# Kernel tuning notes

Measured on AMD Instinct MI355X. Metric: run time of the kernel, lower is better.

Reference implementation:

```python
import jax, jax.numpy as jnp
import numpy as np

N = 50000      # nodes
E = 800000     # edges (avg degree 16)
DIN = 128
DH = 128
DOUT = 40
ALPHA = 0.1
BETA = 1.0


def gcn_conv(x, src, dst, ew, W, b, n):
    """PyG GCNConv: add self-loops, symmetric deg^-1/2 normalization, gather-scatter."""
    idx = jnp.arange(n)
    s = jnp.concatenate([src, idx])
    d = jnp.concatenate([dst, idx])
    w = jnp.concatenate([ew, jnp.ones((n,), x.dtype)])
    deg = jax.ops.segment_sum(w, d, num_segments=n)            # [N]
    dinv = jnp.where(deg > 0, jax.lax.rsqrt(deg), 0.0)
    norm = dinv[s] * w * dinv[d]                               # [E+N]
    h = x @ W                                                  # [N, dout]
    msg = h[s] * norm[:, None]                                 # gather + scale
    out = jax.ops.segment_sum(msg, d, num_segments=n)          # scatter-add
    return out + b


def setup_inputs() -> dict:
    key = jax.random.key(0)
    ks = jax.random.split(key, 10)
    x = jax.random.normal(ks[0], (N, DIN), jnp.float32)
    edge_index = jax.random.randint(ks[1], (2, E), 0, N, dtype=jnp.int64)
    edge_weight = jax.random.uniform(ks[2], (E,), jnp.float32)
    W1 = jax.random.normal(ks[3], (DIN, DH), jnp.float32) / np.float32(np.sqrt(DIN))
    b1 = jnp.zeros((DH,), jnp.float32)
    W2 = jax.random.normal(ks[4], (DH, DH), jnp.float32) / np.float32(np.sqrt(DH))
    b2 = jnp.zeros((DH,), jnp.float32)
    W3 = jax.random.normal(ks[5], (DH, DOUT), jnp.float32) / np.float32(np.sqrt(DH))
    b3 = jnp.zeros((DOUT,), jnp.float32)
    return {"x": x, "edge_index": edge_index, "edge_weight": edge_weight,
            "W1": W1, "b1": b1, "W2": W2, "b2": b2, "W3": W3, "b3": b3}


def reference(x, edge_index, edge_weight, W1, b1, W2, b2, W3, b3):
    src, dst = edge_index[0], edge_index[1]
    ones_w = jnp.ones((E,), x.dtype)
    h1 = jax.nn.relu(gcn_conv(x, src, dst, ones_w, W1, b1, N))   # conv1 (edge_weight=None)
    hc = gcn_conv(h1, src, dst, edge_weight, W2, b2, N)          # crf_layer with edge_weight
    h = ALPHA * h1 + BETA * hc                                   # weighted residual combo
    # LearnableBernoulliDropout: identity in eval mode
    out = gcn_conv(h, src, dst, ones_w, W3, b3, N)               # conv2
    return jax.nn.log_softmax(out, axis=1)
```

## Files before the change

kernel.cpp:

```cpp
#include <hip/hip_runtime.h>
#include <math.h>

#define DIN  128
#define DH   128
#define DOUT 40
#define ALPHA_C 0.1f
#define BETA_C  1.0f
#define NXCD 8
#define PSLOT 16
#define FSLOT 64

typedef __attribute__((ext_vector_type(8))) short short8;
typedef __attribute__((ext_vector_type(4))) float floatx4;

static inline int cdiv_h(int a, int b) { return (a + b - 1) / b; }

static __device__ __forceinline__ unsigned short f2b(float f) {
    unsigned u = __float_as_uint(f);
    u = u + 0x7FFFu + ((u >> 16) & 1u);
    return (unsigned short)(u >> 16);
}
static __device__ __forceinline__ unsigned pk2(float x, float y) {
    return (unsigned)f2b(x) | ((unsigned)f2b(y) << 16);
}
static __device__ __forceinline__ float2 b2f2(unsigned u) {
    float2 r;
    r.x = __uint_as_float(u << 16);
    r.y = __uint_as_float(u & 0xFFFF0000u);
    return r;
}

__global__ __launch_bounds__(256) void build_part(const int* __restrict__ src,
                                                  const int* __restrict__ dst,
                                                  const float* __restrict__ ew,
                                                  int* __restrict__ cnt8,
                                                  int2* __restrict__ csrP, int N, int E) {
    unsigned xcc = __builtin_amdgcn_s_getreg((31u << 11) | 20u) & 7u;
    int quarter = (E + 3) >> 2;
    int e0 = blockIdx.x * 256 + threadIdx.x;
    int* cntp = cnt8 + (size_t)xcc * N;

    int idx[4]; int d[4], s[4]; float w[4]; int pos[4]; bool v[4];
    #pragma unroll
    for (int k = 0; k < 4; ++k) { idx[k] = e0 + k * quarter; v[k] = idx[k] < E; }
    #pragma unroll
    for (int k = 0; k < 4; ++k) if (v[k]) { d[k] = dst[idx[k]]; s[k] = src[idx[k]]; w[k] = ew[idx[k]]; }
    #pragma unroll
    for (int k = 0; k < 4; ++k) if (v[k])
        pos[k] = __hip_atomic_fetch_add(&cntp[d[k]], 1, __ATOMIC_RELAXED, __HIP_MEMORY_SCOPE_WORKGROUP);
    #pragma unroll
    for (int k = 0; k < 4; ++k) if (v[k] && pos[k] < PSLOT - 1) {
        int2 r; r.x = s[k]; r.y = __float_as_int(w[k]);
        csrP[((size_t)d[k] << 7) + (xcc << 4) + pos[k]] = r;
    }
}

__global__ __launch_bounds__(256) void compact(const int* __restrict__ cnt8,
                                               const int2* __restrict__ csrP,
                                               int2* __restrict__ csrF,
                                               int* __restrict__ len,
                                               float* __restrict__ dinv1,
                                               float* __restrict__ dinv2, int N) {
    int row = blockIdx.x * 4 + (threadIdx.x >> 6);
    if (row >= N) return;
    int lane = threadIdx.x & 63;

    int cg[NXCD], pre[NXCD]; int tot = 0;
    #pragma unroll
    for (int g = 0; g < NXCD; ++g) {
        int c = cnt8[(size_t)g * N + row];
        if (c > PSLOT - 1) c = PSLOT - 1;
        cg[g] = c; pre[g] = tot; tot += c;
    }

    float wsum = 0.f;
    #pragma unroll
    for (int h = 0; h < 2; ++h) {
        int slot = lane + 64 * h;
        int g = slot >> 4, pos = slot & 15;
        if (pos < cg[g]) {
            int2 r = csrP[((size_t)row << 7) + slot];
            int dsti = pre[g] + pos;
            if (dsti < FSLOT) csrF[((size_t)row << 6) + dsti] = r;
            wsum += __int_as_float(r.y);
        }
    }
    #pragma unroll
    for (int o = 1; o < 64; o <<= 1) wsum += __shfl_xor(wsum, o, 64);

    if (lane == 0) {
        int t = tot > FSLOT ? FSLOT : tot;
        len[row] = t;
        dinv1[row] = rsqrtf((float)tot + 1.f);
        dinv2[row] = rsqrtf(wsum + 1.f);
    }
}

__global__ __launch_bounds__(256) void wt_conv(const float* __restrict__ W1,
                                               const float* __restrict__ W2,
                                               const float* __restrict__ W3,
                                               unsigned short* __restrict__ WT) {
    int gid = blockIdx.x * 256 + threadIdx.x;
    if (gid < 16384) {
        int n = gid >> 7, k = gid & 127;
        WT[gid] = f2b(W1[(size_t)k * 128 + n]);
    } else if (gid < 32768) {
        int idx = gid - 16384, n = idx >> 7, k = idx & 127;
        WT[gid] = f2b(W2[(size_t)k * 128 + n]);
    } else if (gid < 32768 + 6144) {
        int idx = gid - 32768, n = idx >> 7, k = idx & 127;
        WT[gid] = (n < 40) ? f2b(W3[(size_t)k * 40 + n]) : (unsigned short)0;
    }
}

template <bool ABF16>
__global__ __launch_bounds__(256) void gemm128(const void* __restrict__ Ain,
                                               const unsigned short* __restrict__ WT,
                                               unsigned short* __restrict__ C, int M) {
    __shared__ short As[128 * 128];
    __shared__ short Bs[128 * 128];
    int t = threadIdx.x;
    int blockM = blockIdx.x * 128;
    int r = t >> 1, h = t & 1;

    {
        int rg = blockM + r; if (rg > M - 1) rg = M - 1;
        if (ABF16) {
            const uint4* arow = (const uint4*)((const unsigned short*)Ain + (size_t)rg * 128);
            #pragma unroll
            for (int i = 0; i < 8; ++i) {
                int chunk = h * 8 + i;
                uint4 v = arow[chunk];
                *(uint4*)&As[r * 128 + ((chunk ^ (r & 7)) * 8)] = v;
            }
        } else {
            const float4* arow = (const float4*)((const float*)Ain + (size_t)rg * 128);
            #pragma unroll
            for (int i = 0; i < 8; ++i) {
                int chunk = h * 8 + i;
                float4 v0 = arow[chunk * 2], v1 = arow[chunk * 2 + 1];
                uint4 p;
                p.x = pk2(v0.x, v0.y); p.y = pk2(v0.z, v0.w);
                p.z = pk2(v1.x, v1.y); p.w = pk2(v1.z, v1.w);
                *(uint4*)&As[r * 128 + ((chunk ^ (r & 7)) * 8)] = p;
            }
        }
    }
    {
        const uint4* brow = (const uint4*)(WT + (size_t)r * 128);
        #pragma unroll
        for (int i = 0; i < 8; ++i) {
            int chunk = h * 8 + i;
            uint4 v = brow[chunk];
            *(uint4*)&Bs[r * 128 + ((chunk ^ (r & 7)) * 8)] = v;
        }
    }
    __syncthreads();

    int w = t >> 6, l = t & 63;
    int q = l >> 4, lm = l & 15;
    int rowoff = (w >> 1) * 64, coloff = (w & 1) * 64;

    floatx4 acc[4][4] = {};
    #pragma unroll
    for (int ks = 0; ks < 4; ++ks) {
        int chunk = ks * 4 + q;
        int sw = (chunk ^ (lm & 7)) * 8;
        short8 af[4], bf[4];
        #pragma unroll
        for (int tm = 0; tm < 4; ++tm)
            af[tm] = *(const short8*)&As[(rowoff + tm * 16 + lm) * 128 + sw];
        #pragma unroll
        for (int tn = 0; tn < 4; ++tn)
            bf[tn] = *(const short8*)&Bs[(coloff + tn * 16 + lm) * 128 + sw];
        #pragma unroll
        for (int tm = 0; tm < 4; ++tm)
            #pragma unroll
            for (int tn = 0; tn < 4; ++tn)
                acc[tm][tn] = __builtin_amdgcn_mfma_f32_16x16x32_bf16(af[tm], bf[tn], acc[tm][tn], 0, 0, 0);
    }

    #pragma unroll
    for (int tm = 0; tm < 4; ++tm) {
        #pragma unroll
        for (int reg = 0; reg < 4; ++reg) {
            int row = blockM + rowoff + tm * 16 + q * 4 + reg;
            if (row >= M) continue;
            #pragma unroll
            for (int tn = 0; tn < 4; ++tn) {
                int col = coloff + tn * 16 + lm;
                C[(size_t)row * 128 + col] = f2b(acc[tm][tn][reg]);
            }
        }
    }
}

__global__ __launch_bounds__(256) void gemm40_lsm(const unsigned short* __restrict__ Ain,
                                                  const unsigned short* __restrict__ WT3,
                                                  const float* __restrict__ bias,
                                                  float* __restrict__ out, int M) {
    __shared__ short As[128 * 128];
    __shared__ short Bs[48 * 128];
    int t = threadIdx.x;
    int blockM = blockIdx.x * 128;

    {
        int r = t >> 1, h = t & 1;
        int rg = blockM + r; if (rg > M - 1) rg = M - 1;
        const uint4* arow = (const uint4*)(Ain + (size_t)rg * 128);
        #pragma unroll
        for (int i = 0; i < 8; ++i) {
            int chunk = h * 8 + i;
            uint4 v = arow[chunk];
            *(uint4*)&As[r * 128 + ((chunk ^ (r & 7)) * 8)] = v;
        }
    }
    if (t < 96) {
        int r = t >> 1, h = t & 1;
        const uint4* brow = (const uint4*)(WT3 + (size_t)r * 128);
        #pragma unroll
        for (int i = 0; i < 8; ++i) {
            int chunk = h * 8 + i;
            uint4 v = brow[chunk];
            *(uint4*)&Bs[r * 128 + ((chunk ^ (r & 7)) * 8)] = v;
        }
    }
    __syncthreads();

    int w = t >> 6, l = t & 63;
    int q = l >> 4, lm = l & 15;
    int rowoff = w * 32;

    floatx4 acc[2][3] = {};
    #pragma unroll
    for (int ks = 0; ks < 4; ++ks) {
        int chunk = ks * 4 + q;
        int sw = (chunk ^ (lm & 7)) * 8;
        short8 af[2], bf[3];
        #pragma unroll
        for (int tm = 0; tm < 2; ++tm)
            af[tm] = *(const short8*)&As[(rowoff + tm * 16 + lm) * 128 + sw];
        #pragma unroll
        for (int tn = 0; tn < 3; ++tn)
            bf[tn] = *(const short8*)&Bs[(tn * 16 + lm) * 128 + sw];
        #pragma unroll
        for (int tm = 0; tm < 2; ++tm)
            #pragma unroll
            for (int tn = 0; tn < 3; ++tn)
                acc[tm][tn] = __builtin_amdgcn_mfma_f32_16x16x32_bf16(af[tm], bf[tn], acc[tm][tn], 0, 0, 0);
    }

    float bb0 = bias[lm];
    float bb1 = bias[16 + lm];
    float bb2 = (lm < 8) ? bias[32 + lm] : 0.f;
    #pragma unroll
    for (int tm = 0; tm < 2; ++tm) {
        #pragma unroll
        for (int reg = 0; reg < 4; ++reg) {
            int row = blockM + rowoff + tm * 16 + q * 4 + reg;
            float v0 = acc[tm][0][reg] + bb0;
            float v1 = acc[tm][1][reg] + bb1;
            float v2 = (lm < 8) ? acc[tm][2][reg] + bb2 : -INFINITY;
            float mx = fmaxf(fmaxf(v0, v1), v2);
            #pragma unroll
            for (int o = 1; o < 16; o <<= 1) mx = fmaxf(mx, __shfl_xor(mx, o, 64));
            float ss = expf(v0 - mx) + expf(v1 - mx) + ((lm < 8) ? expf(v2 - mx) : 0.f);
            #pragma unroll
            for (int o = 1; o < 16; o <<= 1) ss += __shfl_xor(ss, o, 64);
            float ls = mx + logf(ss);
            if (row < M) {
                out[(size_t)row * 40 + lm]      = v0 - ls;
                out[(size_t)row * 40 + 16 + lm] = v1 - ls;
                if (lm < 8) out[(size_t)row * 40 + 32 + lm] = v2 - ls;
            }
        }
    }
}

template <int MODE>
__global__ __launch_bounds__(256) void agg128f(const unsigned short* __restrict__ hpre,
                                               unsigned short* __restrict__ io,
                                               const float* __restrict__ bias,
                                               const float* __restrict__ dinv,
                                               const int* __restrict__ len,
                                               const int2* __restrict__ csrF, int n) {
    int row = blockIdx.x * 4 + (threadIdx.x >> 6);
    if (row >= n) return;
    int lane = threadIdx.x & 63;
    const unsigned* hp = (const unsigned*)hpre;

    float di = dinv[row];
    float d2 = di * di;
    float2 acc = b2f2(hp[(size_t)row * 64 + lane]);
    if (MODE == 2) {
        acc.x *= d2; acc.y *= d2;
    } else {
        float2 bb = ((const float2*)bias)[lane];
        acc.x = fmaf(acc.x, d2, bb.x);
        acc.y = fmaf(acc.y, d2, bb.y);
    }

    int c = len[row];
    size_t jb = (size_t)row << 6;
    int j = 0;

    while (j + 8 <= c) {
        int2 ee[8]; float2 ff[8];
        #pragma unroll
        for (int u = 0; u < 8; ++u) ee[u] = csrF[jb + j + u];
        #pragma unroll
        for (int u = 0; u < 8; ++u) ff[u] = b2f2(hp[(size_t)ee[u].x * 64 + lane]);
        #pragma unroll
        for (int u = 0; u < 8; ++u) {
            float cc = (MODE == 1) ? dinv[ee[u].x] * __int_as_float(ee[u].y) * di
                                   : dinv[ee[u].x] * di;
            acc.x = fmaf(cc, ff[u].x, acc.x);
            acc.y = fmaf(cc, ff[u].y, acc.y);
        }
        j += 8;
    }
    if (j + 4 <= c) {
        int2 ee[4]; float2 ff[4];
        #pragma unroll
        for (int u = 0; u < 4; ++u) ee[u] = csrF[jb + j + u];
        #pragma unroll
        for (int u = 0; u < 4; ++u) ff[u] = b2f2(hp[(size_t)ee[u].x * 64 + lane]);
        #pragma unroll
        for (int u = 0; u < 4; ++u) {
            float cc = (MODE == 1) ? dinv[ee[u].x] * __int_as_float(ee[u].y) * di
                                   : dinv[ee[u].x] * di;
            acc.x = fmaf(cc, ff[u].x, acc.x);
            acc.y = fmaf(cc, ff[u].y, acc.y);
        }
        j += 4;
    }
    for (; j < c; ++j) {
        int2 e0 = csrF[jb + j];
        float cc = (MODE == 1) ? dinv[e0.x] * __int_as_float(e0.y) * di : dinv[e0.x] * di;
        float2 f0 = b2f2(hp[(size_t)e0.x * 64 + lane]);
        acc.x = fmaf(cc, f0.x, acc.x);
        acc.y = fmaf(cc, f0.y, acc.y);
    }

    unsigned* iop = (unsigned*)io;
    if (MODE == 0) {
        acc.x = fmaxf(acc.x, 0.f); acc.y = fmaxf(acc.y, 0.f);
        iop[(size_t)row * 64 + lane] = pk2(acc.x, acc.y);
    } else if (MODE == 1) {
        float2 h1 = b2f2(iop[(size_t)row * 64 + lane]);
        acc.x = fmaf(ALPHA_C, h1.x, BETA_C * acc.x);
        acc.y = fmaf(ALPHA_C, h1.y, BETA_C * acc.y);
        iop[(size_t)row * 64 + lane] = pk2(acc.x, acc.y);
    } else {
        iop[(size_t)row * 64 + lane] = pk2(acc.x, acc.y);
    }
}

extern "C" void kernel_launch(void* const* d_in, const int* in_sizes, int n_in,
                              void* d_out, int out_size, void* d_ws, size_t ws_size,
                              hipStream_t stream) {
    const float* x   = (const float*)d_in[0];
    const int*   ei  = (const int*)  d_in[1];
    const float* ew  = (const float*)d_in[2];
    const float* W1  = (const float*)d_in[3];
    const float* b1  = (const float*)d_in[4];
    const float* W2  = (const float*)d_in[5];
    const float* b2  = (const float*)d_in[6];
    const float* W3  = (const float*)d_in[7];
    const float* b3  = (const float*)d_in[8];
    float* out = (float*)d_out;

    const int Nn = in_sizes[0] / DIN;
    const int E  = in_sizes[1] / 2;
    const int* src = ei;
    const int* dst = ei + E;

    char* wsb = (char*)d_ws;
    int*      cnt8  = (int*)wsb;                         wsb += (size_t)NXCD * Nn * 4;
    int*      len   = (int*)wsb;                         wsb += (size_t)Nn * 4;
    float*    dinv1 = (float*)wsb;                       wsb += (size_t)Nn * 4;
    float*    dinv2 = (float*)wsb;                       wsb += (size_t)Nn * 4;
    unsigned short* WT = (unsigned short*)wsb;           wsb += (size_t)(32768 + 6144) * 2;
    int2*     csrF  = (int2*)wsb;                        wsb += (size_t)Nn * FSLOT * 8;
    int2*     csrP  = (int2*)wsb;
    unsigned short* hpreb = (unsigned short*)csrP;
    unsigned short* h1b   = (unsigned short*)csrP + (size_t)Nn * DH;

    hipMemsetAsync(cnt8, 0, (size_t)NXCD * Nn * 4, stream);
    build_part<<<cdiv_h((E + 3) / 4, 256), 256, 0, stream>>>(src, dst, ew, cnt8, csrP, Nn, E);
    compact<<<cdiv_h(Nn, 4), 256, 0, stream>>>(cnt8, csrP, csrF, len, dinv1, dinv2, Nn);
    wt_conv<<<cdiv_h(32768 + 6144, 256), 256, 0, stream>>>(W1, W2, W3, WT);

    int gemmGrid = cdiv_h(Nn, 128);
    int aggGrid = cdiv_h(Nn, 4);

    gemm128<false><<<gemmGrid, 256, 0, stream>>>(x, WT, hpreb, Nn);
    agg128f<0><<<aggGrid, 256, 0, stream>>>(hpreb, h1b, b1, dinv1, len, csrF, Nn);

    gemm128<true><<<gemmGrid, 256, 0, stream>>>(h1b, WT + 16384, hpreb, Nn);
    agg128f<1><<<aggGrid, 256, 0, stream>>>(hpreb, h1b, b2, dinv2, len, csrF, Nn);

    agg128f<2><<<aggGrid, 256, 0, stream>>>(h1b, hpreb, b3, dinv1, len, csrF, Nn);
    gemm40_lsm<<<gemmGrid, 256, 0, stream>>>(hpreb, WT + 32768, b3, out, Nn);
}
```

Baseline: 306.3 us.

## Pack CSR edges to 32-bit, fuse setup kernels, and split rows across half-waves

Each edge record is packed into one 32-bit word: a 16-bit source index plus a bf16 edge weight. This halves the CSR bytes written and read. The weight-transpose kernel is merged into the edge-partition kernel, and the compaction pass is merged into the first GEMM launch as extra blocks, which removes two launches and lets independent work overlap. The aggregation kernel now has each half-wave handle alternate edges with 8-byte feature loads, then combines the halves with a cross-lane shuffle. The 16-bit source index only works while N is at most 65536, and the bf16 weight lowers precision in the CRF normalization.

```diff
diff --git a/kernel.cpp b/kernel.cpp
--- a/kernel.cpp
+++ b/kernel.cpp
@@ -9,6 +9,7 @@
 #define NXCD 8
 #define PSLOT 16
 #define FSLOT 64
+#define WT_TOT (16384 + 16384 + 6144)
 
 typedef __attribute__((ext_vector_type(8))) short short8;
 typedef __attribute__((ext_vector_type(4))) float floatx4;
@@ -30,99 +31,57 @@
     return r;
 }
 
-__global__ __launch_bounds__(256) void build_part(const int* __restrict__ src,
-                                                  const int* __restrict__ dst,
-                                                  const float* __restrict__ ew,
-                                                  int* __restrict__ cnt8,
-                                                  int2* __restrict__ csrP, int N, int E) {
+__global__ __launch_bounds__(256) void build_wt(const int* __restrict__ src,
+                                                const int* __restrict__ dst,
+                                                const float* __restrict__ ew,
+                                                const float* __restrict__ W1,
+                                                const float* __restrict__ W2,
+                                                const float* __restrict__ W3,
+                                                int* __restrict__ cnt8,
+                                                unsigned* __restrict__ csrP,
+                                                unsigned short* __restrict__ WT,
+                                                int N, int E, int buildBlocks) {
+    int b = blockIdx.x;
+    if (b >= buildBlocks) {
+        int gid = (b - buildBlocks) * 256 + threadIdx.x;
+        if (gid < 16384) {
+            int n = gid >> 7, k = gid & 127;
+            WT[gid] = f2b(W1[(size_t)k * 128 + n]);
+        } else if (gid < 32768) {
+            int idx = gid - 16384, n = idx >> 7, k = idx & 127;
+            WT[gid] = f2b(W2[(size_t)k * 128 + n]);
+        } else if (gid < WT_TOT) {
+            int idx = gid - 32768, n = idx >> 7, k = idx & 127;
+            WT[gid] = (n < 40) ? f2b(W3[(size_t)k * 40 + n]) : (unsigned short)0;
+        }
+        return;
+    }
     unsigned xcc = __builtin_amdgcn_s_getreg((31u << 11) | 20u) & 7u;
     int quarter = (E + 3) >> 2;
-    int e0 = blockIdx.x * 256 + threadIdx.x;
+    int e0 = b * 256 + threadIdx.x;
     int* cntp = cnt8 + (size_t)xcc * N;
 
-    int idx[4]; int d[4], s[4]; float w[4]; int pos[4]; bool v[4];
+    int idx[4], d[4]; unsigned rec[4]; int pos[4]; bool v[4];
     #pragma unroll
     for (int k = 0; k < 4; ++k) { idx[k] = e0 + k * quarter; v[k] = idx[k] < E; }
     #pragma unroll
-    for (int k = 0; k < 4; ++k) if (v[k]) { d[k] = dst[idx[k]]; s[k] = src[idx[k]]; w[k] = ew[idx[k]]; }
+    for (int k = 0; k < 4; ++k) if (v[k]) {
+        d[k] = dst[idx[k]];
+        rec[k] = ((unsigned)f2b(ew[idx[k]]) << 16) | ((unsigned)src[idx[k]] & 0xFFFFu);
+    }
     #pragma unroll
     for (int k = 0; k < 4; ++k) if (v[k])
         pos[k] = __hip_atomic_fetch_add(&cntp[d[k]], 1, __ATOMIC_RELAXED, __HIP_MEMORY_SCOPE_WORKGROUP);
     #pragma unroll
-    for (int k = 0; k < 4; ++k) if (v[k] && pos[k] < PSLOT - 1) {
-        int2 r; r.x = s[k]; r.y = __float_as_int(w[k]);
-        csrP[((size_t)d[k] << 7) + (xcc << 4) + pos[k]] = r;
-    }
-}
-
-__global__ __launch_bounds__(256) void compact(const int* __restrict__ cnt8,
-                                               const int2* __restrict__ csrP,
-                                               int2* __restrict__ csrF,
-                                               int* __restrict__ len,
-                                               float* __restrict__ dinv1,
-                                               float* __restrict__ dinv2, int N) {
-    int row = blockIdx.x * 4 + (threadIdx.x >> 6);
-    if (row >= N) return;
-    int lane = threadIdx.x & 63;
-
-    int cg[NXCD], pre[NXCD]; int tot = 0;
-    #pragma unroll
-    for (int g = 0; g < NXCD; ++g) {
-        int c = cnt8[(size_t)g * N + row];
-        if (c > PSLOT - 1) c = PSLOT - 1;
-        cg[g] = c; pre[g] = tot; tot += c;
-    }
-
-    float wsum = 0.f;
-    #pragma unroll
-    for (int h = 0; h < 2; ++h) {
-        int slot = lane + 64 * h;
-        int g = slot >> 4, pos = slot & 15;
-        if (pos < cg[g]) {
-            int2 r = csrP[((size_t)row << 7) + slot];
-            int dsti = pre[g] + pos;
-            if (dsti < FSLOT) csrF[((size_t)row << 6) + dsti] = r;
-            wsum += __int_as_float(r.y);
-        }
-    }
-    #pragma unroll
-    for (int o = 1; o < 64; o <<= 1) wsum += __shfl_xor(wsum, o, 64);
-
-    if (lane == 0) {
-        int t = tot > FSLOT ? FSLOT : tot;
-        len[row] = t;
-        dinv1[row] = rsqrtf((float)tot + 1.f);
-        dinv2[row] = rsqrtf(wsum + 1.f);
-    }
-}
-
-__global__ __launch_bounds__(256) void wt_conv(const float* __restrict__ W1,
-                                               const float* __restrict__ W2,
-                                               const float* __restrict__ W3,
-                                               unsigned short* __restrict__ WT) {
-    int gid = blockIdx.x * 256 + threadIdx.x;
-    if (gid < 16384) {
-        int n = gid >> 7, k = gid & 127;
-        WT[gid] = f2b(W1[(size_t)k * 128 + n]);
-    } else if (gid < 32768) {
-        int idx = gid - 16384, n = idx >> 7, k = idx & 127;
-        WT[gid] = f2b(W2[(size_t)k * 128 + n]);
-    } else if (gid < 32768 + 6144) {
-        int idx = gid - 32768, n = idx >> 7, k = idx & 127;
-        WT[gid] = (n < 40) ? f2b(W3[(size_t)k * 40 + n]) : (unsigned short)0;
-    }
+    for (int k = 0; k < 4; ++k) if (v[k] && pos[k] < PSLOT - 1)
+        csrP[((size_t)d[k] << 7) + (xcc << 4) + pos[k]] = rec[k];
 }
 
 template <bool ABF16>
-__global__ __launch_bounds__(256) void gemm128(const void* __restrict__ Ain,
-                                               const unsigned short* __restrict__ WT,
-                                               unsigned short* __restrict__ C, int M) {
-    __shared__ short As[128 * 128];
-    __shared__ short Bs[128 * 128];
-    int t = threadIdx.x;
-    int blockM = blockIdx.x * 128;
+static __device__ __forceinline__ void gemm128_body(short* As, short* Bs,
+        const void* __restrict__ Ain, const unsigned short* __restrict__ WT,
+        unsigned short* __restrict__ C, int M, int blockM, int t) {
     int r = t >> 1, h = t & 1;
-
     {
         int rg = blockM + r; if (rg > M - 1) rg = M - 1;
         if (ABF16) {
@@ -195,6 +154,64 @@
     }
 }
 
+template <bool ABF16>
+__global__ __launch_bounds__(256) void gemm128(const void* __restrict__ Ain,
+                                               const unsigned short* __restrict__ WT,
+                                               unsigned short* __restrict__ C, int M) {
+    __shared__ short As[128 * 128];
+    __shared__ short Bs[128 * 128];
+    gemm128_body<ABF16>(As, Bs, Ain, WT, C, M, blockIdx.x * 128, threadIdx.x);
+}
+
+__global__ __launch_bounds__(256) void gemm1_compact(const float* __restrict__ x,
+                                                     const unsigned short* __restrict__ WT,
+                                                     unsigned short* __restrict__ C, int M,
+                                                     const int* __restrict__ cnt8,
+                                                     const unsigned* __restrict__ csrP,
+                                                     unsigned* __restrict__ csrF,
+                                                     int* __restrict__ len,
+                                                     float* __restrict__ dinv1,
+                                                     float* __restrict__ dinv2,
+                                                     int N, int gemmBlocks) {
+    __shared__ short As[128 * 128];
+    __shared__ short Bs[128 * 128];
+    if ((int)blockIdx.x < gemmBlocks) {
+        gemm128_body<false>(As, Bs, x, WT, C, M, blockIdx.x * 128, threadIdx.x);
+        return;
+    }
+    int bid = blockIdx.x - gemmBlocks;
+    int row = bid * 4 + (threadIdx.x >> 6);
+    if (row >= N) return;
+    int lane = threadIdx.x & 63;
+
+    int cg[NXCD], pre[NXCD]; int tot = 0;
+    #pragma unroll
+    for (int g = 0; g < NXCD; ++g) {
+        int c = cnt8[(size_t)g * N + row];
+        if (c > PSLOT - 1) c = PSLOT - 1;
+        cg[g] = c; pre[g] = tot; tot += c;
+    }
+    float wsum = 0.f;
+    #pragma unroll
+    for (int h2 = 0; h2 < 2; ++h2) {
+        int slot = lane + 64 * h2;
+        int g = slot >> 4, pos = slot & 15;
+        if (pos < cg[g]) {
+            unsigned rec = csrP[((size_t)row << 7) + slot];
+            int dsti = pre[g] + pos;
+            if (dsti < FSLOT) csrF[((size_t)row << 6) + dsti] = rec;
+            wsum += __uint_as_float(rec & 0xFFFF0000u);
+        }
+    }
+    #pragma unroll
+    for (int o = 1; o < 64; o <<= 1) wsum += __shfl_xor(wsum, o, 64);
+    if (lane == 0) {
+        len[row] = tot > FSLOT ? FSLOT : tot;
+        dinv1[row] = rsqrtf((float)tot + 1.f);
+        dinv2[row] = rsqrtf(wsum + 1.f);
+    }
+}
+
 __global__ __launch_bounds__(256) void gemm40_lsm(const unsigned short* __restrict__ Ain,
                                                   const unsigned short* __restrict__ WT3,
                                                   const float* __restrict__ bias,
@@ -278,81 +295,95 @@
 }
 
 template <int MODE>
+static __device__ __forceinline__ void edge_acc(unsigned e, uint2 v, float di,
+                                                const float* __restrict__ dinv, float4& acc) {
+    int s = e & 0xFFFFu;
+    float cc = (MODE == 1) ? dinv[s] * __uint_as_float(e & 0xFFFF0000u) * di
+                           : dinv[s] * di;
+    float2 p0 = b2f2(v.x), p1 = b2f2(v.y);
+    acc.x = fmaf(cc, p0.x, acc.x); acc.y = fmaf(cc, p0.y, acc.y);
+    acc.z = fmaf(cc, p1.x, acc.z); acc.w = fmaf(cc, p1.y, acc.w);
+}
+
+template <int MODE>
 __global__ __launch_bounds__(256) void agg128f(const unsigned short* __restrict__ hpre,
                                                unsigned short* __restrict__ io,
                                                const float* __restrict__ bias,
                                                const float* __restrict__ dinv,
                                                const int* __restrict__ len,
-                                               const int2* __restrict__ csrF, int n) {
+                                               const unsigned* __restrict__ csrF, int n) {
     int row = blockIdx.x * 4 + (threadIdx.x >> 6);
     if (row >= n) return;
     int lane = threadIdx.x & 63;
-    const unsigned* hp = (const unsigned*)hpre;
+    int sub = lane >> 5, ch = lane & 31;
+    const uint2* hp2 = (const uint2*)hpre;
 
     float di = dinv[row];
-    float d2 = di * di;
-    float2 acc = b2f2(hp[(size_t)row * 64 + lane]);
-    if (MODE == 2) {
-        acc.x *= d2; acc.y *= d2;
-    } else {
-        float2 bb = ((const float2*)bias)[lane];
-        acc.x = fmaf(acc.x, d2, bb.x);
-        acc.y = fmaf(acc.y, d2, bb.y);
-    }
+    float4 acc = {0.f, 0.f, 0.f, 0.f};
 
     int c = len[row];
     size_t jb = (size_t)row << 6;
     int j = 0;
 
-    while (j + 8 <= c) {
-        int2 ee[8]; float2 ff[8];
-        #pragma unroll
-        for (int u = 0; u < 8; ++u) ee[u] = csrF[jb + j + u];
-        #pragma unroll
-        for (int u = 0; u < 8; ++u) ff[u] = b2f2(hp[(size_t)ee[u].x * 64 + lane]);
-        #pragma unroll
-        for (int u = 0; u < 8; ++u) {
-            float cc = (MODE == 1) ? dinv[ee[u].x] * __int_as_float(ee[u].y) * di
-                                   : dinv[ee[u].x] * di;
-            acc.x = fmaf(cc, ff[u].x, acc.x);
-            acc.y = fmaf(cc, ff[u].y, acc.y);
-        }
+    while (j + 16 <= c) {
+        unsigned e[8]; uint2 v[8];
+        #pragma unroll
+        for (int u = 0; u < 8; ++u) e[u] = csrF[jb + j + 2 * u + sub];
+        #pragma unroll
+        for (int u = 0; u < 8; ++u) v[u] = hp2[(size_t)(e[u] & 0xFFFFu) * 32 + ch];
+        #pragma unroll
+        for (int u = 0; u < 8; ++u) edge_acc<MODE>(e[u], v[u], di, dinv, acc);
+        j += 16;
+    }
+    if (j + 8 <= c) {
+        unsigned e[4]; uint2 v[4];
+        #pragma unroll
+        for (int u = 0; u < 4; ++u) e[u] = csrF[jb + j + 2 * u + sub];
+        #pragma unroll
+        for (int u = 0; u < 4; ++u) v[u] = hp2[(size_t)(e[u] & 0xFFFFu) * 32 + ch];
+        #pragma unroll
+        for (int u = 0; u < 4; ++u) edge_acc<MODE>(e[u], v[u], di, dinv, acc);
         j += 8;
     }
-    if (j + 4 <= c) {
-        int2 ee[4]; float2 ff[4];
-        #pragma unroll
-        for (int u = 0; u < 4; ++u) ee[u] = csrF[jb + j + u];
-        #pragma unroll
-        for (int u = 0; u < 4; ++u) ff[u] = b2f2(hp[(size_t)ee[u].x * 64 + lane]);
-        #pragma unroll
-        for (int u = 0; u < 4; ++u) {
-            float cc = (MODE == 1) ? dinv[ee[u].x] * __int_as_float(ee[u].y) * di
-                                   : dinv[ee[u].x] * di;
-            acc.x = fmaf(cc, ff[u].x, acc.x);
-            acc.y = fmaf(cc, ff[u].y, acc.y);
-        }
-        j += 4;
-    }
-    for (; j < c; ++j) {
-        int2 e0 = csrF[jb + j];
-        float cc = (MODE == 1) ? dinv[e0.x] * __int_as_float(e0.y) * di : dinv[e0.x] * di;
-        float2 f0 = b2f2(hp[(size_t)e0.x * 64 + lane]);
-        acc.x = fmaf(cc, f0.x, acc.x);
-        acc.y = fmaf(cc, f0.y, acc.y);
-    }
-
-    unsigned* iop = (unsigned*)io;
-    if (MODE == 0) {
-        acc.x = fmaxf(acc.x, 0.f); acc.y = fmaxf(acc.y, 0.f);
-        iop[(size_t)row * 64 + lane] = pk2(acc.x, acc.y);
-    } else if (MODE == 1) {
-        float2 h1 = b2f2(iop[(size_t)row * 64 + lane]);
-        acc.x = fmaf(ALPHA_C, h1.x, BETA_C * acc.x);
-        acc.y = fmaf(ALPHA_C, h1.y, BETA_C * acc.y);
-        iop[(size_t)row * 64 + lane] = pk2(acc.x, acc.y);
-    } else {
-        iop[(size_t)row * 64 + lane] = pk2(acc.x, acc.y);
+    for (; j < c; j += 2) {
+        if (j + sub < c) {
+            unsigned e0 = csrF[jb + j + sub];
+            uint2 v0 = hp2[(size_t)(e0 & 0xFFFFu) * 32 + ch];
+            edge_acc<MODE>(e0, v0, di, dinv, acc);
+        }
+    }
+
+    acc.x += __shfl_xor(acc.x, 32, 64);
+    acc.y += __shfl_xor(acc.y, 32, 64);
+    acc.z += __shfl_xor(acc.z, 32, 64);
+    acc.w += __shfl_xor(acc.w, 32, 64);
+
+    if (sub == 0) {
+        float d2 = di * di;
+        uint2 self = hp2[(size_t)row * 32 + ch];
+        float2 s0 = b2f2(self.x), s1 = b2f2(self.y);
+        float v0 = fmaf(s0.x, d2, acc.x);
+        float v1 = fmaf(s0.y, d2, acc.y);
+        float v2 = fmaf(s1.x, d2, acc.z);
+        float v3 = fmaf(s1.y, d2, acc.w);
+        uint2* iop = (uint2*)io + (size_t)row * 32 + ch;
+        if (MODE != 2) {
+            float4 bb = ((const float4*)bias)[ch];
+            v0 += bb.x; v1 += bb.y; v2 += bb.z; v3 += bb.w;
+        }
+        if (MODE == 0) {
+            v0 = fmaxf(v0, 0.f); v1 = fmaxf(v1, 0.f);
+            v2 = fmaxf(v2, 0.f); v3 = fmaxf(v3, 0.f);
+        } else if (MODE == 1) {
+            uint2 h1 = *iop;
+            float2 a0 = b2f2(h1.x), a1 = b2f2(h1.y);
+            v0 = fmaf(ALPHA_C, a0.x, BETA_C * v0);
+            v1 = fmaf(ALPHA_C, a0.y, BETA_C * v1);
+            v2 = fmaf(ALPHA_C, a1.x, BETA_C * v2);
+            v3 = fmaf(ALPHA_C, a1.y, BETA_C * v3);
+        }
+        uint2 o; o.x = pk2(v0, v1); o.y = pk2(v2, v3);
+        *iop = o;
     }
 }
 
@@ -380,21 +411,24 @@
     int*      len   = (int*)wsb;                         wsb += (size_t)Nn * 4;
     float*    dinv1 = (float*)wsb;                       wsb += (size_t)Nn * 4;
     float*    dinv2 = (float*)wsb;                       wsb += (size_t)Nn * 4;
-    unsigned short* WT = (unsigned short*)wsb;           wsb += (size_t)(32768 + 6144) * 2;
-    int2*     csrF  = (int2*)wsb;                        wsb += (size_t)Nn * FSLOT * 8;
-    int2*     csrP  = (int2*)wsb;
-    unsigned short* hpreb = (unsigned short*)csrP;
-    unsigned short* h1b   = (unsigned short*)csrP + (size_t)Nn * DH;
+    unsigned short* WT = (unsigned short*)wsb;           wsb += (size_t)WT_TOT * 2;
+    unsigned* csrP  = (unsigned*)wsb;                    wsb += (size_t)Nn * 128 * 4;
+    unsigned* csrF  = (unsigned*)wsb;                    wsb += (size_t)Nn * FSLOT * 4;
+    unsigned short* hpreb = (unsigned short*)wsb;        wsb += (size_t)Nn * DH * 2;
+    unsigned short* h1b   = (unsigned short*)wsb;        wsb += (size_t)Nn * DH * 2;
+
+    const int buildBlocks = cdiv_h((E + 3) / 4, 256);
+    const int wtBlocks    = cdiv_h(WT_TOT, 256);
+    const int gemmGrid    = cdiv_h(Nn, 128);
+    const int aggGrid     = cdiv_h(Nn, 4);
 
     hipMemsetAsync(cnt8, 0, (size_t)NXCD * Nn * 4, stream);
-    build_part<<<cdiv_h((E + 3) / 4, 256), 256, 0, stream>>>(src, dst, ew, cnt8, csrP, Nn, E);
-    compact<<<cdiv_h(Nn, 4), 256, 0, stream>>>(cnt8, csrP, csrF, len, dinv1, dinv2, Nn);
-    wt_conv<<<cdiv_h(32768 + 6144, 256), 256, 0, stream>>>(W1, W2, W3, WT);
-
-    int gemmGrid = cdiv_h(Nn, 128);
-    int aggGrid = cdiv_h(Nn, 4);
-
-    gemm128<false><<<gemmGrid, 256, 0, stream>>>(x, WT, hpreb, Nn);
+    build_wt<<<buildBlocks + wtBlocks, 256, 0, stream>>>(src, dst, ew, W1, W2, W3,
+                                                         cnt8, csrP, WT, Nn, E, buildBlocks);
+    gemm1_compact<<<gemmGrid + aggGrid, 256, 0, stream>>>(x, WT, hpreb, Nn,
+                                                          cnt8, csrP, csrF, len, dinv1, dinv2,
+                                                          Nn, gemmGrid);
+
     agg128f<0><<<aggGrid, 256, 0, stream>>>(hpreb, h1b, b1, dinv1, len, csrF, Nn);
 
     gemm128<true><<<gemmGrid, 256, 0, stream>>>(h1b, WT + 16384, hpreb, Nn);
```

After: 326.6 us. 1.07x slower.
